# Kernel tuning notes

Measured on AMD Instinct MI355X. Metric: run time of the kernel, lower is better.

The kernel has to match this reference:

```python
import jax, jax.numpy as jnp
import numpy as np

HIDDEN_DIM = 64
EIGS_DIM = 16
N_LAYERS = 2
NUM_USERS = 100000
NUM_ITEMS = 200000
N_NODES = NUM_USERS + NUM_ITEMS
N_EDGES = 1250000
N_PATHS = 14  # 2**(sample_hop+1) - 2 with sample_hop=3
LN_EPS = 1e-5


def setup_inputs() -> dict:
    key = jax.random.key(0)
    k1, k2, k3, k4, k5 = jax.random.split(key, 5)
    return {
        "user_emb": 0.1 * jax.random.normal(k1, (NUM_USERS, HIDDEN_DIM), dtype=jnp.float32),
        "item_emb": 0.1 * jax.random.normal(k2, (NUM_ITEMS, HIDDEN_DIM), dtype=jnp.float32),
        "eigs": jax.random.normal(k3, (N_NODES, EIGS_DIM), dtype=jnp.float32),
        "lambda0": jnp.zeros((N_LAYERS,), dtype=jnp.float32),
        "path_emb_w": jnp.zeros((N_LAYERS, N_PATHS, 1), dtype=jnp.float32),
        "indices": jax.random.randint(k4, (2, N_EDGES), 0, N_NODES, dtype=jnp.int64)
        if jax.config.jax_enable_x64
        else jax.random.randint(k4, (2, N_EDGES), 0, N_NODES, dtype=jnp.int32),
        "path_type": jax.random.randint(k5, (N_EDGES,), 0, N_PATHS, dtype=jnp.int32),
    }


def _layer_norm(x, eps=LN_EPS):
    mu = jnp.mean(x, axis=-1, keepdims=True)
    var = jnp.var(x, axis=-1, keepdims=True)
    return (x - mu) * jax.lax.rsqrt(var + eps)


def _sparse_softmax(row, s, num_nodes):
    # softmax over edges grouped by target-node row index
    m = jax.ops.segment_max(s, row, num_segments=num_nodes)
    e = jnp.exp(s - m[row])
    denom = jax.ops.segment_sum(e, row, num_segments=num_nodes)
    return e / denom[row]


def _attention(y, eigs, row, col, path_type, lam0, pemb):
    sqrt_dim = 1.0 / jnp.sqrt(jnp.float32(HIDDEN_DIM))
    # per-edge q.k score  [E]
    x = jnp.sum(y[row] * y[col], axis=-1) * sqrt_dim
    yeig = jnp.sum(eigs[row] * eigs[col], axis=-1)
    s0 = x + jnp.exp(lam0) * yeig
    s1 = pemb[path_type, 0]
    a0 = _sparse_softmax(row, s0, N_NODES)
    a1 = _sparse_softmax(row, s1, N_NODES)
    a = 0.5 * (a0 + a1)
    # sparse-dense matmul: out[r] = sum_e a_e * v[col_e]
    return jax.ops.segment_sum(a[:, None] * y[col], row, num_segments=N_NODES)


def reference(user_emb, item_emb, eigs, lambda0, path_emb_w, indices, path_type):
    row, col = indices[0], indices[1]
    all_emb = jnp.concatenate([user_emb, item_emb], axis=0)  # [N, d]
    embs = [all_emb]
    for l in range(N_LAYERS):
        y = _layer_norm(all_emb)
        all_emb = _attention(y, eigs, row, col, path_type, lambda0[l], path_emb_w[l])
        embs.append(all_emb)
    light_out = jnp.mean(jnp.stack(embs, axis=1), axis=1)  # [N, d]
    return light_out
```

## Files before the change

### kernel.cpp

```cpp
#include <hip/hip_runtime.h>
#include <hip/hip_bf16.h>

#define HD 64
#define ED 16
#define NU 100000
#define NI 200000
#define NN 300000
#define NE 1250000
#define NP 14

#define RB 512
#define NBKT ((NN + RB - 1) / RB)
#define A_ITEMS 8
#define A_CHUNK (256 * A_ITEMS)
#define A_BLOCKS ((NE + A_CHUNK - 1) / A_CHUNK)

typedef __hip_bfloat16 bf16;
typedef unsigned short ushort8v __attribute__((ext_vector_type(8)));

__device__ __forceinline__ float bf2f(unsigned short u) {
    union { unsigned int i; float f; } c; c.i = ((unsigned int)u) << 16; return c.f;
}
__device__ __forceinline__ unsigned short f2b(float x) {
    bf16 h = __float2bfloat16(x);
    unsigned short u; __builtin_memcpy(&u, &h, 2); return u;
}

__global__ void ln_kernel(const float* __restrict__ user_emb,
                          const float* __restrict__ item_emb,
                          bf16* __restrict__ yb)
{
    const int wave = (int)((blockIdx.x * blockDim.x + threadIdx.x) >> 6);
    const int lane = (int)(threadIdx.x & 63);
    if (wave >= NN) return;
    const size_t idx = (size_t)wave * HD + lane;
    const float x = (wave < NU) ? user_emb[idx] : item_emb[idx - (size_t)NU * HD];

    float s = x, sq = x * x;
#pragma unroll
    for (int o = 32; o; o >>= 1) {
        s  += __shfl_xor(s, o, 64);
        sq += __shfl_xor(sq, o, 64);
    }
    const float mu  = s * (1.0f / 64.0f);
    const float var = sq * (1.0f / 64.0f) - mu * mu;
    yb[idx] = __float2bfloat16((x - mu) * rsqrtf(var + 1e-5f));
}

__global__ void bkt_count_kernel(const int* __restrict__ row,
                                 int* __restrict__ bkt_cnt)
{
    __shared__ int hist[NBKT];
    const int tid = threadIdx.x;
    for (int j = tid; j < NBKT; j += 256) hist[j] = 0;
    __syncthreads();
    const int base = blockIdx.x * A_CHUNK;
#pragma unroll
    for (int i = 0; i < A_ITEMS; ++i) {
        const int idx = base + i * 256 + tid;
        if (idx < NE) atomicAdd(&hist[row[idx] >> 9], 1);
    }
    __syncthreads();
    for (int j = tid; j < NBKT; j += 256) {
        const int h = hist[j];
        if (h) atomicAdd(&bkt_cnt[j], h);
    }
}

__global__ void bkt_scan_kernel(const int* __restrict__ bkt_cnt,
                                int* __restrict__ bkt_base,
                                int* __restrict__ wq_bkt)
{
    __shared__ int s[1024];
    const int t = threadIdx.x;
    const int v = (t < NBKT) ? bkt_cnt[t] : 0;
    s[t] = v;
    __syncthreads();
    for (int off = 1; off < 1024; off <<= 1) {
        int x = (t >= off) ? s[t - off] : 0;
        __syncthreads();
        s[t] += x;
        __syncthreads();
    }
    if (t < NBKT) {
        const int excl = s[t] - v;
        bkt_base[t] = excl;
        wq_bkt[t]   = excl;
        if (t == NBKT - 1) bkt_base[NBKT] = s[t];
    }
}

__global__ void bkt_scatter_kernel(const int* __restrict__ row,
                                   const int* __restrict__ col,
                                   const int* __restrict__ pt,
                                   int* __restrict__ wq_bkt,
                                   int* __restrict__ pairs)
{
    __shared__ int hist[NBKT];
    __shared__ int rbase[NBKT];
    __shared__ int roff[NBKT];
    const int tid = threadIdx.x;
    for (int j = tid; j < NBKT; j += 256) { hist[j] = 0; roff[j] = 0; }
    __syncthreads();

    const int base = blockIdx.x * A_CHUNK;
    int vals[A_ITEMS], bkts[A_ITEMS];
#pragma unroll
    for (int i = 0; i < A_ITEMS; ++i) {
        const int idx = base + i * 256 + tid;
        bkts[i] = -1;
        if (idx < NE) {
            const int r = row[idx];
            vals[i] = col[idx] | (pt[idx] << 19) | ((r & (RB - 1)) << 23);
            bkts[i] = r >> 9;
            atomicAdd(&hist[bkts[i]], 1);
        }
    }
    __syncthreads();
    for (int j = tid; j < NBKT; j += 256) {
        const int h = hist[j];
        if (h) rbase[j] = atomicAdd(&wq_bkt[j], h);
    }
    __syncthreads();
#pragma unroll
    for (int i = 0; i < A_ITEMS; ++i) {
        if (bkts[i] >= 0) {
            const int o = atomicAdd(&roff[bkts[i]], 1);
            pairs[rbase[bkts[i]] + o] = vals[i];
        }
    }
}

__global__ void bkt_sort_kernel(const int* __restrict__ bkt_base,
                                const int* __restrict__ pairs,
                                const float* __restrict__ eigs,
                                int* __restrict__ rowptr,
                                int* __restrict__ cnt,
                                int2* __restrict__ epacked)
{
    __shared__ int rcnt[RB], lrp[RB], wq2[RB], ssum[256];
    __shared__ float estage[RB * ED];
    const int tid = threadIdx.x;
    const int b   = blockIdx.x;
    const int r0  = b * RB;
    const int s   = bkt_base[b];
    const int e   = bkt_base[b + 1];

    for (int j = tid; j < RB; j += 256) { rcnt[j] = 0; wq2[j] = 0; }
    for (int k = tid; k < RB * ED; k += 256) {
        const int g = r0 * ED + k;
        estage[k] = (g < NN * ED) ? eigs[g] : 0.0f;
    }
    __syncthreads();

    for (int i = s + tid; i < e; i += 256)
        atomicAdd(&rcnt[(pairs[i] >> 23) & (RB - 1)], 1);
    __syncthreads();

    const int a0 = rcnt[2 * tid], a1 = rcnt[2 * tid + 1];
    ssum[tid] = a0 + a1;
    __syncthreads();
    for (int off = 1; off < 256; off <<= 1) {
        int x = (tid >= off) ? ssum[tid - off] : 0;
        __syncthreads();
        ssum[tid] += x;
        __syncthreads();
    }
    const int excl = ssum[tid] - (a0 + a1);
    lrp[2 * tid]     = excl;
    lrp[2 * tid + 1] = excl + a0;
    {
        const int r = r0 + 2 * tid;
        if (r < NN)     { rowptr[r]     = s + excl;      cnt[r]     = a0; }
        if (r + 1 < NN) { rowptr[r + 1] = s + excl + a0; cnt[r + 1] = a1; }
    }
    __syncthreads();

    for (int i = s + tid; i < e; i += 256) {
        const int v  = pairs[i];
        const int rl = (v >> 23) & (RB - 1);
        const int c  = v & 0x7FFFF;
        const float4* ep = (const float4*)(eigs + (size_t)c * ED);
        const float4 q0 = ep[0], q1 = ep[1], q2 = ep[2], q3 = ep[3];
        const float* er = estage + rl * ED;
        float d = q0.x * er[0]  + q0.y * er[1]  + q0.z * er[2]  + q0.w * er[3]
                + q1.x * er[4]  + q1.y * er[5]  + q1.z * er[6]  + q1.w * er[7]
                + q2.x * er[8]  + q2.y * er[9]  + q2.z * er[10] + q2.w * er[11]
                + q3.x * er[12] + q3.y * er[13] + q3.z * er[14] + q3.w * er[15];
        const int o   = atomicAdd(&wq2[rl], 1);
        const int pos = s + lrp[rl] + o;
        epacked[pos] = make_int2(v & 0x7FFFFF, __float_as_int(d));
    }
}

template <int LAYER>
__global__ void attn_row_kernel(const bf16* __restrict__ yb,
                                const int* __restrict__ rowptr,
                                const int* __restrict__ cnt,
                                const int2* __restrict__ epacked,
                                const float* __restrict__ lambda0,
                                const float* __restrict__ pemb,
                                const float* __restrict__ user_emb,
                                const float* __restrict__ item_emb,
                                bf16* __restrict__ yb_next,
                                float* __restrict__ io)
{
    __shared__ float e1tab[NP];
    if (threadIdx.x < NP)
        e1tab[threadIdx.x] = __expf(pemb[LAYER * NP + threadIdx.x]);
    __syncthreads();

    const int tid  = blockIdx.x * blockDim.x + threadIdx.x;
    const int r    = tid >> 3;
    const int sub  = tid & 7;
    const int lane = (int)(threadIdx.x & 63);
    if (r >= NN) return;
    const int deg = cnt[r];
    if (LAYER == 1 && deg == 0) return;

    const int start = rowptr[r];
    const float lam = __expf(lambda0[LAYER]);

    float yrf[8];
    {
        ushort8v u = *reinterpret_cast<const ushort8v*>(yb + (size_t)r * HD + sub * 8);
#pragma unroll
        for (int j = 0; j < 8; ++j) yrf[j] = bf2f(u[j]);
    }

    float U0[8], U1[8];
#pragma unroll
    for (int j = 0; j < 8; ++j) { U0[j] = 0.0f; U1[j] = 0.0f; }
    float d0 = 0.0f, d1 = 0.0f;

    int2 myv = (sub < deg) ? epacked[start + sub] : make_int2(0, 0);
    for (int k = 0; k < deg; ++k) {
        const int kk = k & 7;
        if (k && kk == 0)
            myv = (k + sub < deg) ? epacked[start + k + sub] : make_int2(0, 0);
        const int src = (lane & ~7) + kk;
        const int   v    = __shfl(myv.x, src, 64);
        const float edot = __int_as_float(__shfl(myv.y, src, 64));
        const int c = v & 0x7FFFF;
        const int p = (v >> 19) & 15;

        ushort8v uc = *reinterpret_cast<const ushort8v*>(yb + (size_t)c * HD + sub * 8);
        float yc[8];
        float sdot = 0.0f;
#pragma unroll
        for (int j = 0; j < 8; ++j) { yc[j] = bf2f(uc[j]); sdot += yrf[j] * yc[j]; }
        sdot += __shfl_xor(sdot, 1, 64);
        sdot += __shfl_xor(sdot, 2, 64);
        sdot += __shfl_xor(sdot, 4, 64);

        const float e0 = __expf(sdot * 0.125f + lam * edot);
        const float e1 = e1tab[p];
        d0 += e0; d1 += e1;
#pragma unroll
        for (int j = 0; j < 8; ++j) {
            U0[j] += e0 * yc[j];
            U1[j] += e1 * yc[j];
        }
    }

    const float i0 = deg ? 0.5f / d0 : 0.0f;
    const float i1 = deg ? 0.5f / d1 : 0.0f;
    float acc[8];
#pragma unroll
    for (int j = 0; j < 8; ++j) acc[j] = i0 * U0[j] + i1 * U1[j];

    float* iorow = io + (size_t)r * HD + sub * 8;
    if (LAYER == 0) {
        float sm = 0.0f, sq = 0.0f;
#pragma unroll
        for (int j = 0; j < 8; ++j) { sm += acc[j]; sq += acc[j] * acc[j]; }
        sm += __shfl_xor(sm, 1, 64); sq += __shfl_xor(sq, 1, 64);
        sm += __shfl_xor(sm, 2, 64); sq += __shfl_xor(sq, 2, 64);
        sm += __shfl_xor(sm, 4, 64); sq += __shfl_xor(sq, 4, 64);
        const float mu  = sm * (1.0f / 64.0f);
        const float var = sq * (1.0f / 64.0f) - mu * mu;
        const float inv = rsqrtf(var + 1e-5f);
        ushort8v w;
#pragma unroll
        for (int j = 0; j < 8; ++j) w[j] = f2b((acc[j] - mu) * inv);
        *reinterpret_cast<ushort8v*>(yb_next + (size_t)r * HD + sub * 8) = w;

        const float* e0p = (r < NU) ? user_emb + (size_t)r * HD + sub * 8
                                    : item_emb + (size_t)(r - NU) * HD + sub * 8;
        const float4 lo = *reinterpret_cast<const float4*>(e0p);
        const float4 hi = *reinterpret_cast<const float4*>(e0p + 4);
        const float third = 1.0f / 3.0f;
        *reinterpret_cast<float4*>(iorow) =
            make_float4((lo.x + acc[0]) * third, (lo.y + acc[1]) * third,
                        (lo.z + acc[2]) * third, (lo.w + acc[3]) * third);
        *reinterpret_cast<float4*>(iorow + 4) =
            make_float4((hi.x + acc[4]) * third, (hi.y + acc[5]) * third,
                        (hi.z + acc[6]) * third, (hi.w + acc[7]) * third);
    } else {
        const float third = 1.0f / 3.0f;
        float4 lo = *reinterpret_cast<const float4*>(iorow);
        float4 hi = *reinterpret_cast<const float4*>(iorow + 4);
        lo.x += acc[0] * third; lo.y += acc[1] * third;
        lo.z += acc[2] * third; lo.w += acc[3] * third;
        hi.x += acc[4] * third; hi.y += acc[5] * third;
        hi.z += acc[6] * third; hi.w += acc[7] * third;
        *reinterpret_cast<float4*>(iorow)     = lo;
        *reinterpret_cast<float4*>(iorow + 4) = hi;
    }
}

extern "C" void kernel_launch(void* const* d_in, const int* in_sizes, int n_in,
                              void* d_out, int out_size, void* d_ws, size_t ws_size,
                              hipStream_t stream)
{
    const float* user_emb = (const float*)d_in[0];
    const float* item_emb = (const float*)d_in[1];
    const float* eigs     = (const float*)d_in[2];
    const float* lambda0  = (const float*)d_in[3];
    const float* pemb     = (const float*)d_in[4];
    const int*   indices  = (const int*)d_in[5];
    const int*   ptype    = (const int*)d_in[6];
    const int*   row = indices;
    const int*   col = indices + NE;

    float* io = (float*)d_out;
    char*  ws = (char*)d_ws;
    bf16* yb       = (bf16*)ws;
    bf16* yb2      = yb + (size_t)NN * HD;
    int*  pairs    = (int*)(yb2 + (size_t)NN * HD);
    int2* epacked  = (int2*)(pairs + NE);
    int*  rowptr   = (int*)(epacked + NE);
    int*  cnt      = rowptr + NN;
    int*  bkt_cnt  = cnt + NN;
    int*  bkt_base = bkt_cnt + NBKT;
    int*  wq_bkt   = bkt_base + NBKT + 1;

    const dim3 blk(256);
    const int ln_grid   = (NN * 64) / 256;
    const int attn_grid = (NN * 8) / 256;

    hipMemsetAsync(bkt_cnt, 0, NBKT * sizeof(int), stream);
    bkt_count_kernel<<<A_BLOCKS, blk, 0, stream>>>(row, bkt_cnt);
    bkt_scan_kernel<<<1, 1024, 0, stream>>>(bkt_cnt, bkt_base, wq_bkt);
    bkt_scatter_kernel<<<A_BLOCKS, blk, 0, stream>>>(row, col, ptype, wq_bkt, pairs);
    bkt_sort_kernel<<<NBKT, blk, 0, stream>>>(bkt_base, pairs, eigs,
                                              rowptr, cnt, epacked);

    ln_kernel<<<ln_grid, blk, 0, stream>>>(user_emb, item_emb, yb);
    attn_row_kernel<0><<<attn_grid, blk, 0, stream>>>(yb, rowptr, cnt, epacked,
                                                      lambda0, pemb, user_emb,
                                                      item_emb, yb2, io);
    attn_row_kernel<1><<<attn_grid, blk, 0, stream>>>(yb2, rowptr, cnt, epacked,
                                                      lambda0, pemb, user_emb,
                                                      item_emb, nullptr, io);
}
```

Baseline: 414.0 us.

## Gather bf16 eigenvectors in sort, vectorize layernorm, rebalance scatter chunking

The layernorm kernel now has 8 threads per row using float4 loads and 16-byte bf16 stores. It also writes a bf16 copy of the eigenvector table and runs before the bucket sort. The sort kernel gathers the column-side eigenvectors from that bf16 copy, halving the bytes of its random gathers, but the eigenvector dot product now uses reduced precision on one side. The scatter kernel re-reads row, col and ptype in its second pass instead of holding them in registers, and items per block double, which cuts register pressure at the cost of extra reads.

```diff
diff --git a/kernel.cpp b/kernel.cpp
--- a/kernel.cpp
+++ b/kernel.cpp
@@ -11,7 +11,7 @@
 
 #define RB 512
 #define NBKT ((NN + RB - 1) / RB)
-#define A_ITEMS 8
+#define A_ITEMS 16
 #define A_CHUNK (256 * A_ITEMS)
 #define A_BLOCKS ((NE + A_CHUNK - 1) / A_CHUNK)
 
@@ -28,23 +28,38 @@
 
 __global__ void ln_kernel(const float* __restrict__ user_emb,
                           const float* __restrict__ item_emb,
-                          bf16* __restrict__ yb)
-{
-    const int wave = (int)((blockIdx.x * blockDim.x + threadIdx.x) >> 6);
-    const int lane = (int)(threadIdx.x & 63);
-    if (wave >= NN) return;
-    const size_t idx = (size_t)wave * HD + lane;
-    const float x = (wave < NU) ? user_emb[idx] : item_emb[idx - (size_t)NU * HD];
-
-    float s = x, sq = x * x;
-#pragma unroll
-    for (int o = 32; o; o >>= 1) {
-        s  += __shfl_xor(s, o, 64);
-        sq += __shfl_xor(sq, o, 64);
-    }
-    const float mu  = s * (1.0f / 64.0f);
+                          const float* __restrict__ eigs,
+                          bf16* __restrict__ yb,
+                          bf16* __restrict__ eb)
+{
+    const int tid = blockIdx.x * blockDim.x + threadIdx.x;
+    const int r   = tid >> 3;
+    const int sub = tid & 7;
+    if (r >= NN) return;
+    const float* src = (r < NU) ? user_emb + (size_t)r * HD
+                                : item_emb + (size_t)(r - NU) * HD;
+    const float4 lo = *reinterpret_cast<const float4*>(src + sub * 8);
+    const float4 hi = *reinterpret_cast<const float4*>(src + sub * 8 + 4);
+    float x[8] = {lo.x, lo.y, lo.z, lo.w, hi.x, hi.y, hi.z, hi.w};
+
+    float sm = 0.0f, sq = 0.0f;
+#pragma unroll
+    for (int j = 0; j < 8; ++j) { sm += x[j]; sq += x[j] * x[j]; }
+    sm += __shfl_xor(sm, 1, 64); sq += __shfl_xor(sq, 1, 64);
+    sm += __shfl_xor(sm, 2, 64); sq += __shfl_xor(sq, 2, 64);
+    sm += __shfl_xor(sm, 4, 64); sq += __shfl_xor(sq, 4, 64);
+    const float mu  = sm * (1.0f / 64.0f);
     const float var = sq * (1.0f / 64.0f) - mu * mu;
-    yb[idx] = __float2bfloat16((x - mu) * rsqrtf(var + 1e-5f));
+    const float inv = rsqrtf(var + 1e-5f);
+
+    ushort8v w;
+#pragma unroll
+    for (int j = 0; j < 8; ++j) w[j] = f2b((x[j] - mu) * inv);
+    *reinterpret_cast<ushort8v*>(yb + (size_t)r * HD + sub * 8) = w;
+
+    const float2 ev = *reinterpret_cast<const float2*>(eigs + (size_t)r * ED + sub * 2);
+    const unsigned int packed = (unsigned int)f2b(ev.x) | ((unsigned int)f2b(ev.y) << 16);
+    *reinterpret_cast<unsigned int*>(eb + (size_t)r * ED + sub * 2) = packed;
 }
 
 __global__ void bkt_count_kernel(const int* __restrict__ row,
@@ -104,17 +119,10 @@
     __syncthreads();
 
     const int base = blockIdx.x * A_CHUNK;
-    int vals[A_ITEMS], bkts[A_ITEMS];
 #pragma unroll
     for (int i = 0; i < A_ITEMS; ++i) {
         const int idx = base + i * 256 + tid;
-        bkts[i] = -1;
-        if (idx < NE) {
-            const int r = row[idx];
-            vals[i] = col[idx] | (pt[idx] << 19) | ((r & (RB - 1)) << 23);
-            bkts[i] = r >> 9;
-            atomicAdd(&hist[bkts[i]], 1);
-        }
+        if (idx < NE) atomicAdd(&hist[row[idx] >> 9], 1);
     }
     __syncthreads();
     for (int j = tid; j < NBKT; j += 256) {
@@ -124,9 +132,13 @@
     __syncthreads();
 #pragma unroll
     for (int i = 0; i < A_ITEMS; ++i) {
-        if (bkts[i] >= 0) {
-            const int o = atomicAdd(&roff[bkts[i]], 1);
-            pairs[rbase[bkts[i]] + o] = vals[i];
+        const int idx = base + i * 256 + tid;
+        if (idx < NE) {
+            const int r = row[idx];
+            const int b = r >> 9;
+            const int v = col[idx] | (pt[idx] << 19) | ((r & (RB - 1)) << 23);
+            const int o = atomicAdd(&roff[b], 1);
+            pairs[rbase[b] + o] = v;
         }
     }
 }
@@ -134,6 +146,7 @@
 __global__ void bkt_sort_kernel(const int* __restrict__ bkt_base,
                                 const int* __restrict__ pairs,
                                 const float* __restrict__ eigs,
+                                const bf16* __restrict__ eb,
                                 int* __restrict__ rowptr,
                                 int* __restrict__ cnt,
                                 int2* __restrict__ epacked)
@@ -180,13 +193,14 @@
         const int v  = pairs[i];
         const int rl = (v >> 23) & (RB - 1);
         const int c  = v & 0x7FFFF;
-        const float4* ep = (const float4*)(eigs + (size_t)c * ED);
-        const float4 q0 = ep[0], q1 = ep[1], q2 = ep[2], q3 = ep[3];
+        const ushort8v* ep = reinterpret_cast<const ushort8v*>(eb + (size_t)c * ED);
+        const ushort8v q0 = ep[0], q1 = ep[1];
         const float* er = estage + rl * ED;
-        float d = q0.x * er[0]  + q0.y * er[1]  + q0.z * er[2]  + q0.w * er[3]
-                + q1.x * er[4]  + q1.y * er[5]  + q1.z * er[6]  + q1.w * er[7]
-                + q2.x * er[8]  + q2.y * er[9]  + q2.z * er[10] + q2.w * er[11]
-                + q3.x * er[12] + q3.y * er[13] + q3.z * er[14] + q3.w * er[15];
+        float d = 0.0f;
+#pragma unroll
+        for (int j = 0; j < 8; ++j) d += bf2f(q0[j]) * er[j];
+#pragma unroll
+        for (int j = 0; j < 8; ++j) d += bf2f(q1[j]) * er[j + 8];
         const int o   = atomicAdd(&wq2[rl], 1);
         const int pos = s + lrp[rl] + o;
         epacked[pos] = make_int2(v & 0x7FFFFF, __float_as_int(d));
@@ -327,7 +341,8 @@
     char*  ws = (char*)d_ws;
     bf16* yb       = (bf16*)ws;
     bf16* yb2      = yb + (size_t)NN * HD;
-    int*  pairs    = (int*)(yb2 + (size_t)NN * HD);
+    bf16* eb       = yb2 + (size_t)NN * HD;
+    int*  pairs    = (int*)(eb + (size_t)NN * ED);
     int2* epacked  = (int2*)(pairs + NE);
     int*  rowptr   = (int*)(epacked + NE);
     int*  cnt      = rowptr + NN;
@@ -336,21 +351,21 @@
     int*  wq_bkt   = bkt_base + NBKT + 1;
 
     const dim3 blk(256);
-    const int ln_grid   = (NN * 64) / 256;
-    const int attn_grid = (NN * 8) / 256;
+    const int grid8 = (NN * 8) / 256;
+
+    ln_kernel<<<grid8, blk, 0, stream>>>(user_emb, item_emb, eigs, yb, eb);
 
     hipMemsetAsync(bkt_cnt, 0, NBKT * sizeof(int), stream);
     bkt_count_kernel<<<A_BLOCKS, blk, 0, stream>>>(row, bkt_cnt);
     bkt_scan_kernel<<<1, 1024, 0, stream>>>(bkt_cnt, bkt_base, wq_bkt);
     bkt_scatter_kernel<<<A_BLOCKS, blk, 0, stream>>>(row, col, ptype, wq_bkt, pairs);
-    bkt_sort_kernel<<<NBKT, blk, 0, stream>>>(bkt_base, pairs, eigs,
+    bkt_sort_kernel<<<NBKT, blk, 0, stream>>>(bkt_base, pairs, eigs, eb,
                                               rowptr, cnt, epacked);
 
-    ln_kernel<<<ln_grid, blk, 0, stream>>>(user_emb, item_emb, yb);
-    attn_row_kernel<0><<<attn_grid, blk, 0, stream>>>(yb, rowptr, cnt, epacked,
-                                                      lambda0, pemb, user_emb,
-                                                      item_emb, yb2, io);
-    attn_row_kernel<1><<<attn_grid, blk, 0, stream>>>(yb2, rowptr, cnt, epacked,
-                                                      lambda0, pemb, user_emb,
-                                                      item_emb, nullptr, io);
-}
+    attn_row_kernel<0><<<grid8, blk, 0, stream>>>(yb, rowptr, cnt, epacked,
+                                                  lambda0, pemb, user_emb,
+                                                  item_emb, yb2, io);
+    attn_row_kernel<1><<<grid8, blk, 0, stream>>>(yb2, rowptr, cnt, epacked,
+                                                  lambda0, pemb, user_emb,
+                                                  item_emb, nullptr, io);
+}
```

Result: faster. 381.0 us (-8.0%).
